# Kernel tuning notes

Hardware: AMD Instinct MI355X
Metric: run time of the kernel (lower is better)

The kernel has to match this reference:

```python
import jax, jax.numpy as jnp
import numpy as np

IN, OUT, HID = 1024, 1024, 2048
L = IN + OUT + HID
EPS = 1e-12  # F.normalize default eps


def _make_strength_matrix():
    fwd_s, bwd_s, lat_s, self_s = 1.0, 0.5, 0.3, 0.0
    i = np.arange(L)
    # torch: triu (incl diag) = forward, then tril (incl diag) = backward -> diag ends up backward here
    A = np.where(i[:, None] >= i[None, :], bwd_s, fwd_s).astype(np.float32)
    # lateral blocks (within input, within output, within hidden)
    A[0:IN, 0:IN] = lat_s
    A[IN:IN + OUT, IN:IN + OUT] = lat_s
    A[IN + OUT:L, IN + OUT:L] = lat_s
    A[i, i] = self_s
    return A


def setup_inputs() -> dict:
    key = jax.random.key(0)
    kx, ky, kw = jax.random.split(key, 3)
    B = 1024
    x = jax.random.normal(kx, (B, IN), dtype=jnp.float32)
    y = jax.random.normal(ky, (B, OUT), dtype=jnp.float32)
    W = jax.random.normal(kw, (L, L), dtype=jnp.float32) * 0.01
    idx = jnp.arange(L)
    W = W.at[idx, idx].set(0.0)  # fill_diagonal_(0) at init
    A = jnp.asarray(_make_strength_matrix())
    return {"x": x, "y": y, "W": W, "A": A, "n": 32}


def reference(x, y, W, A, n):
    # clamp_x=True, clamp_y=False, norm_hidden=True, average_window<=0
    B = x.shape[0]
    act0 = jnp.concatenate(
        [x, jnp.zeros_like(y), jnp.zeros((B, HID), dtype=x.dtype)], axis=1
    )  # [B, L]
    mw = W * A.T  # modified weights, loop-invariant

    def step(act, _):
        act = jax.nn.relu(act @ mw.T)          # linear(act, mw) + relu
        act = act.at[:, :IN].set(x)            # clamp_x
        hid = act[:, IN + OUT:]
        nrm = jnp.linalg.norm(hid, axis=1, keepdims=True)
        hid = hid / jnp.maximum(nrm, EPS)      # F.normalize p=2 dim=1
        act = act.at[:, IN + OUT:].set(hid)
        return act, None

    act, _ = jax.lax.scan(step, act0, None, length=n)
    return act
```

## Files before the change

kernel.cpp:

```cpp
#include <hip/hip_runtime.h>
#include <stdint.h>
#include <stddef.h>


#define L 4096
#define INX 1024
#define OUTX 1024
#define BATCH 1024
#define NCOL 3072
#define NITER 32

#define BM 64
#define BN 96
#define BK 64

typedef float floatx4 __attribute__((ext_vector_type(4)));
typedef short bf16x8 __attribute__((ext_vector_type(8)));

__device__ __forceinline__ unsigned short f2bf(float f) {
  unsigned int u = __float_as_uint(f);
  u += 0x7FFF + ((u >> 16) & 1);
  return (unsigned short)(u >> 16);
}
__device__ __forceinline__ float bf2f(unsigned short h) {
  return __uint_as_float(((unsigned int)h) << 16);
}

__device__ __forceinline__ void load_lds_16B(const void* g, void* s) {
  __builtin_amdgcn_global_load_lds(
      (const __attribute__((address_space(1))) unsigned int*)g,
      (__attribute__((address_space(3))) unsigned int*)s, 16, 0, 0);
}

__global__ void prep_mwn(const float* __restrict__ W, unsigned short* __restrict__ mwn) {
  int idx = blockIdx.x * 256 + threadIdx.x;
  int i = idx >> 10;
  int j4 = (idx & 1023) << 2;
  const float4 w = *(const float4*)&W[(size_t)(INX + i) * L + j4];
  const int c = INX + i;
  const int rc = (c < 2048) ? 1 : 2;
  float wv[4] = {w.x, w.y, w.z, w.w};
  unsigned short o[4];
#pragma unroll
  for (int k = 0; k < 4; ++k) {
    int j = j4 + k;
    int rj = (j < 1024) ? 0 : ((j < 2048) ? 1 : 2);
    float a = (j == c) ? 0.0f : ((rj == rc) ? 0.3f : ((j >= c) ? 0.5f : 1.0f));
    o[k] = f2bf(wv[k] * a);
  }
  *(ushort4*)&mwn[(size_t)i * L + j4] = make_ushort4(o[0], o[1], o[2], o[3]);
}

__global__ void init_act(const float* __restrict__ x, unsigned short* __restrict__ actA) {
  int i = blockIdx.x * 256 + threadIdx.x;
  int col = i & (L - 1), row = i >> 12;
  actA[i] = (col < INX) ? f2bf(x[(size_t)row * INX + col]) : (unsigned short)0;
}

__device__ __forceinline__ void stage(unsigned short* As, unsigned short* Bs,
                                      const unsigned short* gA, const unsigned short* gB,
                                      int kb, int t) {
  const int srow = t >> 3, schunk = t & 7;
  const int o = srow * BK + schunk * 8;
  load_lds_16B(gA + kb, &As[o]);
  load_lds_16B(gA + (size_t)32 * L + kb, &As[o + 32 * BK]);
  load_lds_16B(gB + kb, &Bs[o]);
  load_lds_16B(gB + (size_t)32 * L + kb, &Bs[o + 32 * BK]);
  load_lds_16B(gB + (size_t)64 * L + kb, &Bs[o + 64 * BK]);
}

__device__ __forceinline__ void mfma_step(const unsigned short* As, const unsigned short* Bs,
                                          int wm, int wn, int l15, int quad,
                                          floatx4 acc[2][3]) {
#pragma unroll
  for (int kk = 0; kk < 2; ++kk) {
    bf16x8 af[2], bfr[3];
    const int c = kk * 4 + quad;
#pragma unroll
    for (int mt = 0; mt < 2; ++mt) {
      int r = wm + mt * 16 + l15;
      af[mt] = *(const bf16x8*)&As[r * BK + ((c ^ (r & 7)) * 8)];
    }
#pragma unroll
    for (int nt = 0; nt < 3; ++nt) {
      int r = wn + nt * 16 + l15;
      bfr[nt] = *(const bf16x8*)&Bs[r * BK + ((c ^ (r & 7)) * 8)];
    }
#pragma unroll
    for (int mt = 0; mt < 2; ++mt)
#pragma unroll
      for (int nt = 0; nt < 3; ++nt)
        acc[mt][nt] = __builtin_amdgcn_mfma_f32_16x16x32_bf16(af[mt], bfr[nt],
                                                              acc[mt][nt], 0, 0, 0);
  }
}

#define PSTEP(s, R, D, ACC)                                                       \
  do {                                                                            \
    if ((s) < NS - 1) asm volatile("s_waitcnt vmcnt(5)" ::: "memory");            \
    else              asm volatile("s_waitcnt vmcnt(0)" ::: "memory");            \
    asm volatile("s_barrier" ::: "memory");                                       \
    if ((s) + 2 < NS) stage(As##D, Bs##D, gA, gB, KB0 + ((s) + 2) * BK, t);       \
    mfma_step(As##R, Bs##R, wm, wn, l15, quad, ACC);                              \
  } while (0)

template<int MODE>
__global__ __launch_bounds__(256, 2) void gemm_k(
    const unsigned short* __restrict__ act,
    const unsigned short* __restrict__ mwn,
    unsigned short* __restrict__ actn,
    unsigned short* __restrict__ c0,
    const float* __restrict__ nsq_prev,
    float* __restrict__ nsq_next) {
  __shared__ alignas(16) unsigned short As0[BM * BK], As1[BM * BK], As2[BM * BK];
  __shared__ alignas(16) unsigned short Bs0[BN * BK], Bs1[BN * BK], Bs2[BN * BK];
  const int t = threadIdx.x;
  const int lane = t & 63;
  const int wave = t >> 6;
  const int wm = (wave & 1) * 32;
  const int wn = (wave >> 1) * 48;
  const int l15 = lane & 15;
  const int quad = lane >> 4;

  const int b = blockIdx.y * 32 + blockIdx.x;
  const int n_idx = (b & 7) * 4 + (b >> 7);
  const int m_idx = (b >> 3) & 15;
  const int m0 = m_idx * BM;
  const int n0 = n_idx * BN;

  const int srow = t >> 3;
  const int schunk = t & 7;
  const int gchunk = schunk ^ (srow & 7);
  const unsigned short* gA = act + (size_t)(m0 + srow) * L + gchunk * 8;
  const unsigned short* gB = mwn + (size_t)(n0 + srow) * L + gchunk * 8;

  const int KB0 = MODE ? INX : 0;
  constexpr int NS = MODE ? 48 : 16;

  floatx4 accA[2][3], accB[2][3];
#pragma unroll
  for (int i = 0; i < 2; ++i)
#pragma unroll
    for (int j = 0; j < 3; ++j) {
      accA[i][j] = (floatx4){0.f, 0.f, 0.f, 0.f};
      if (MODE) accB[i][j] = (floatx4){0.f, 0.f, 0.f, 0.f};
    }

  stage(As0, Bs0, gA, gB, KB0, t);
  stage(As1, Bs1, gA, gB, KB0 + BK, t);

  PSTEP(0, 0, 2, accA);  PSTEP(1, 1, 0, accA);  PSTEP(2, 2, 1, accA);
  PSTEP(3, 0, 2, accA);  PSTEP(4, 1, 0, accA);  PSTEP(5, 2, 1, accA);
  PSTEP(6, 0, 2, accA);  PSTEP(7, 1, 0, accA);  PSTEP(8, 2, 1, accA);
  PSTEP(9, 0, 2, accA);  PSTEP(10, 1, 0, accA); PSTEP(11, 2, 1, accA);
  PSTEP(12, 0, 2, accA); PSTEP(13, 1, 0, accA); PSTEP(14, 2, 1, accA);
  PSTEP(15, 0, 2, accA);
  if (MODE) {
    PSTEP(16, 1, 0, accB); PSTEP(17, 2, 1, accB); PSTEP(18, 0, 2, accB);
    PSTEP(19, 1, 0, accB); PSTEP(20, 2, 1, accB); PSTEP(21, 0, 2, accB);
    PSTEP(22, 1, 0, accB); PSTEP(23, 2, 1, accB); PSTEP(24, 0, 2, accB);
    PSTEP(25, 1, 0, accB); PSTEP(26, 2, 1, accB); PSTEP(27, 0, 2, accB);
    PSTEP(28, 1, 0, accB); PSTEP(29, 2, 1, accB); PSTEP(30, 0, 2, accB);
    PSTEP(31, 1, 0, accB); PSTEP(32, 2, 1, accB); PSTEP(33, 0, 2, accB);
    PSTEP(34, 1, 0, accB); PSTEP(35, 2, 1, accB); PSTEP(36, 0, 2, accB);
    PSTEP(37, 1, 0, accB); PSTEP(38, 2, 1, accB); PSTEP(39, 0, 2, accB);
    PSTEP(40, 1, 0, accB); PSTEP(41, 2, 1, accB); PSTEP(42, 0, 2, accB);
    PSTEP(43, 1, 0, accB); PSTEP(44, 2, 1, accB); PSTEP(45, 0, 2, accB);
    PSTEP(46, 1, 0, accB); PSTEP(47, 2, 1, accB);
  }

  if (MODE == 0) {
#pragma unroll
    for (int mt = 0; mt < 2; ++mt)
#pragma unroll
      for (int nt = 0; nt < 3; ++nt) {
        const int gn = n0 + wn + nt * 16 + l15;
#pragma unroll
        for (int r = 0; r < 4; ++r) {
          const int gm = m0 + wm + mt * 16 + quad * 4 + r;
          c0[(size_t)gm * NCOL + gn] = f2bf(accA[mt][nt][r]);
        }
      }
    return;
  }

  float sm[2][4];
#pragma unroll
  for (int mt = 0; mt < 2; ++mt)
#pragma unroll
    for (int r = 0; r < 4; ++r) {
      const int gm = m0 + wm + mt * 16 + quad * 4 + r;
      sm[mt][r] = 1.0f / fmaxf(sqrtf(nsq_prev[gm]), 1e-12f);
    }

  const bool has_hid = (n0 + BN) > OUTX;
#pragma unroll
  for (int mt = 0; mt < 2; ++mt) {
    float ss[4] = {0.f, 0.f, 0.f, 0.f};
#pragma unroll
    for (int nt = 0; nt < 3; ++nt) {
      const int gn = n0 + wn + nt * 16 + l15;
      const bool hid = gn >= OUTX;
#pragma unroll
      for (int r = 0; r < 4; ++r) {
        const int gm = m0 + wm + mt * 16 + quad * 4 + r;
        float v = bf2f(c0[(size_t)gm * NCOL + gn]) + accA[mt][nt][r]
                  + sm[mt][r] * accB[mt][nt][r];
        v = fmaxf(v, 0.f);
        actn[(size_t)gm * L + INX + gn] = f2bf(v);
        if (hid) ss[r] += v * v;
      }
    }
    if (has_hid) {
#pragma unroll
      for (int r = 0; r < 4; ++r) {
        float sv = ss[r];
        sv += __shfl_xor(sv, 1);
        sv += __shfl_xor(sv, 2);
        sv += __shfl_xor(sv, 4);
        sv += __shfl_xor(sv, 8);
        if (l15 == 0)
          atomicAdd(&nsq_next[m0 + wm + mt * 16 + quad * 4 + r], sv);
      }
    }
  }
}

__global__ void finalize(const float* __restrict__ x, const unsigned short* __restrict__ act,
                         const float* __restrict__ nsq_fin, float* __restrict__ out) {
  int i = blockIdx.x * 256 + threadIdx.x;
  int col = i & (L - 1), row = i >> 12;
  float v;
  if (col < INX) {
    v = x[(size_t)row * INX + col];
  } else {
    v = bf2f(act[i]);
    if (col >= INX + OUTX) v *= 1.0f / fmaxf(sqrtf(nsq_fin[row]), 1e-12f);
  }
  out[i] = v;
}

extern "C" void kernel_launch(void* const* d_in, const int* in_sizes, int n_in,
                              void* d_out, int out_size, void* d_ws, size_t ws_size,
                              hipStream_t stream) {
  const float* x = (const float*)d_in[0];
  const float* W = (const float*)d_in[2];
  float* out = (float*)d_out;

  char* ws = (char*)d_ws;
  unsigned short* mwn  = (unsigned short*)(ws);
  unsigned short* actA = (unsigned short*)(ws + 25165824);
  unsigned short* actB = (unsigned short*)(ws + 33554432);
  unsigned short* c0   = (unsigned short*)(ws + 41943040);
  float* normsq        = (float*)(ws + 48234496);

  hipMemsetAsync(normsq, 0, (NITER + 1) * BATCH * sizeof(float), stream);
  prep_mwn<<<(NCOL * (L / 4)) / 256, 256, 0, stream>>>(W, mwn);
  init_act<<<(BATCH * L) / 256, 256, 0, stream>>>(x, actA);

  gemm_k<0><<<dim3(NCOL / BN, BATCH / BM), 256, 0, stream>>>(actA, mwn, nullptr, c0,
                                                             nullptr, nullptr);

  unsigned short* cur = actA;
  unsigned short* nxt = actB;
  for (int it = 0; it < NITER; ++it) {
    gemm_k<1><<<dim3(NCOL / BN, BATCH / BM), 256, 0, stream>>>(
        cur, mwn, nxt, c0, normsq + it * BATCH, normsq + (it + 1) * BATCH);
    unsigned short* tmp = cur; cur = nxt; nxt = tmp;
  }
  finalize<<<(BATCH * L) / 256, 256, 0, stream>>>(x, cur, normsq + NITER * BATCH, out);
}
```

Measured before the change: 1.089 ms.

## Load B operand directly from global into registers, bypassing LDS staging

Each wave now reads its weight (B) fragments straight from global memory into registers in MFMA layout, and only the activation (A) tile is staged through triple-buffered LDS. This removes B's LDS writes and reads and cuts shared-memory use from about 61 KB to about 24 KB per block. The waitcnt is lowered because only two async loads per stage remain. In exchange, the B loads are issued in the same step that consumes them with no prefetch, so global latency is exposed. B rows are also fetched separately by the two waves that share them, which doubles that traffic through the cache.

```diff
diff --git a/kernel.cpp b/kernel.cpp
--- a/kernel.cpp
+++ b/kernel.cpp
@@ -57,51 +57,57 @@
   actA[i] = (col < INX) ? f2bf(x[(size_t)row * INX + col]) : (unsigned short)0;
 }
 
-__device__ __forceinline__ void stage(unsigned short* As, unsigned short* Bs,
-                                      const unsigned short* gA, const unsigned short* gB,
-                                      int kb, int t) {
-  const int srow = t >> 3, schunk = t & 7;
-  const int o = srow * BK + schunk * 8;
+__device__ __forceinline__ void stageA(unsigned short* As, const unsigned short* gA,
+                                       int kb, int t) {
+  const int o = (t >> 3) * BK + (t & 7) * 8;
   load_lds_16B(gA + kb, &As[o]);
   load_lds_16B(gA + (size_t)32 * L + kb, &As[o + 32 * BK]);
-  load_lds_16B(gB + kb, &Bs[o]);
-  load_lds_16B(gB + (size_t)32 * L + kb, &Bs[o + 32 * BK]);
-  load_lds_16B(gB + (size_t)64 * L + kb, &Bs[o + 64 * BK]);
-}
-
-__device__ __forceinline__ void mfma_step(const unsigned short* As, const unsigned short* Bs,
-                                          int wm, int wn, int l15, int quad,
-                                          floatx4 acc[2][3]) {
+}
+
+__device__ __forceinline__ void loadB(bf16x8 b[2][3], const unsigned short* gB0,
+                                      const unsigned short* gB1, const unsigned short* gB2,
+                                      int kb) {
 #pragma unroll
   for (int kk = 0; kk < 2; ++kk) {
-    bf16x8 af[2], bfr[3];
-    const int c = kk * 4 + quad;
+    b[kk][0] = *(const bf16x8*)(gB0 + kb + kk * 32);
+    b[kk][1] = *(const bf16x8*)(gB1 + kb + kk * 32);
+    b[kk][2] = *(const bf16x8*)(gB2 + kb + kk * 32);
+  }
+}
+
+__device__ __forceinline__ void loadA(bf16x8 a[2][2], const unsigned short* As,
+                                      int wm, int l15, int quad) {
+#pragma unroll
+  for (int kk = 0; kk < 2; ++kk)
 #pragma unroll
     for (int mt = 0; mt < 2; ++mt) {
       int r = wm + mt * 16 + l15;
-      af[mt] = *(const bf16x8*)&As[r * BK + ((c ^ (r & 7)) * 8)];
-    }
-#pragma unroll
-    for (int nt = 0; nt < 3; ++nt) {
-      int r = wn + nt * 16 + l15;
-      bfr[nt] = *(const bf16x8*)&Bs[r * BK + ((c ^ (r & 7)) * 8)];
-    }
+      a[kk][mt] = *(const bf16x8*)&As[r * BK + ((((kk * 4 + quad)) ^ (r & 7)) * 8)];
+    }
+}
+
+__device__ __forceinline__ void domfma(const bf16x8 a[2][2], const bf16x8 b[2][3],
+                                       floatx4 acc[2][3]) {
+#pragma unroll
+  for (int kk = 0; kk < 2; ++kk)
 #pragma unroll
     for (int mt = 0; mt < 2; ++mt)
 #pragma unroll
       for (int nt = 0; nt < 3; ++nt)
-        acc[mt][nt] = __builtin_amdgcn_mfma_f32_16x16x32_bf16(af[mt], bfr[nt],
+        acc[mt][nt] = __builtin_amdgcn_mfma_f32_16x16x32_bf16(a[kk][mt], b[kk][nt],
                                                               acc[mt][nt], 0, 0, 0);
-  }
 }
 
 #define PSTEP(s, R, D, ACC)                                                       \
   do {                                                                            \
-    if ((s) < NS - 1) asm volatile("s_waitcnt vmcnt(5)" ::: "memory");            \
+    if ((s) < NS - 1) asm volatile("s_waitcnt vmcnt(2)" ::: "memory");            \
     else              asm volatile("s_waitcnt vmcnt(0)" ::: "memory");            \
     asm volatile("s_barrier" ::: "memory");                                       \
-    if ((s) + 2 < NS) stage(As##D, Bs##D, gA, gB, KB0 + ((s) + 2) * BK, t);       \
-    mfma_step(As##R, Bs##R, wm, wn, l15, quad, ACC);                              \
+    bf16x8 bf[2][3], af[2][2];                                                    \
+    loadB(bf, gB0, gB1, gB2, KB0 + (s) * BK);                                     \
+    loadA(af, As##R, wm, l15, quad);                                              \
+    if ((s) + 2 < NS) stageA(As##D, gA, KB0 + ((s) + 2) * BK, t);                 \
+    domfma(af, bf, ACC);                                                          \
   } while (0)
 
 template<int MODE>
@@ -113,7 +119,6 @@
     const float* __restrict__ nsq_prev,
     float* __restrict__ nsq_next) {
   __shared__ alignas(16) unsigned short As0[BM * BK], As1[BM * BK], As2[BM * BK];
-  __shared__ alignas(16) unsigned short Bs0[BN * BK], Bs1[BN * BK], Bs2[BN * BK];
   const int t = threadIdx.x;
   const int lane = t & 63;
   const int wave = t >> 6;
@@ -129,10 +134,12 @@
   const int n0 = n_idx * BN;
 
   const int srow = t >> 3;
-  const int schunk = t & 7;
-  const int gchunk = schunk ^ (srow & 7);
+  const int gchunk = (t & 7) ^ (srow & 7);
   const unsigned short* gA = act + (size_t)(m0 + srow) * L + gchunk * 8;
-  const unsigned short* gB = mwn + (size_t)(n0 + srow) * L + gchunk * 8;
+
+  const unsigned short* gB0 = mwn + (size_t)(n0 + wn + 0 + l15) * L + quad * 8;
+  const unsigned short* gB1 = mwn + (size_t)(n0 + wn + 16 + l15) * L + quad * 8;
+  const unsigned short* gB2 = mwn + (size_t)(n0 + wn + 32 + l15) * L + quad * 8;
 
   const int KB0 = MODE ? INX : 0;
   constexpr int NS = MODE ? 48 : 16;
@@ -146,8 +153,8 @@
       if (MODE) accB[i][j] = (floatx4){0.f, 0.f, 0.f, 0.f};
     }
 
-  stage(As0, Bs0, gA, gB, KB0, t);
-  stage(As1, Bs1, gA, gB, KB0 + BK, t);
+  stageA(As0, gA, KB0, t);
+  stageA(As1, gA, KB0 + BK, t);
 
   PSTEP(0, 0, 2, accA);  PSTEP(1, 1, 0, accA);  PSTEP(2, 2, 1, accA);
   PSTEP(3, 0, 2, accA);  PSTEP(4, 1, 0, accA);  PSTEP(5, 2, 1, accA);
```

Result: slower. 2.678 ms (+146.0%).

## Double M tile and split K across wave halves with LDS reduction

Applied to the files above, without the earlier changes.

The GEMM block tile grows from 64x96 to 128x96 and uses 512 threads. The two halves of the waves each take half of every K-slice, and their partial accumulators are summed through shared memory at the end. This raises operand reuse per staged tile and halves the grid to 256 blocks, one per CU, to cut redundant loads of the weight matrix. In exchange it adds LDS reduction passes with extra barriers and lowers occupancy to one block per CU.

```diff
diff --git a/kernel.cpp b/kernel.cpp
--- a/kernel.cpp
+++ b/kernel.cpp
@@ -10,7 +10,7 @@
 #define NCOL 3072
 #define NITER 32
 
-#define BM 64
+#define BM 128
 #define BN 96
 #define BK 64
 
@@ -60,94 +60,102 @@
 __device__ __forceinline__ void stage(unsigned short* As, unsigned short* Bs,
                                       const unsigned short* gA, const unsigned short* gB,
                                       int kb, int t) {
-  const int srow = t >> 3, schunk = t & 7;
-  const int o = srow * BK + schunk * 8;
-  load_lds_16B(gA + kb, &As[o]);
-  load_lds_16B(gA + (size_t)32 * L + kb, &As[o + 32 * BK]);
-  load_lds_16B(gB + kb, &Bs[o]);
-  load_lds_16B(gB + (size_t)32 * L + kb, &Bs[o + 32 * BK]);
-  load_lds_16B(gB + (size_t)64 * L + kb, &Bs[o + 64 * BK]);
+  const int o = t * 8;
+  load_lds_16B(gA + kb, As + o);
+  load_lds_16B(gA + (size_t)64 * L + kb, As + 4096 + o);
+  load_lds_16B(gB + kb, Bs + o);
+  if (t < 256)
+    load_lds_16B(gB + (size_t)64 * L + kb, Bs + 4096 + o);
 }
 
 __device__ __forceinline__ void mfma_step(const unsigned short* As, const unsigned short* Bs,
-                                          int wm, int wn, int l15, int quad,
-                                          floatx4 acc[2][3]) {
-#pragma unroll
-  for (int kk = 0; kk < 2; ++kk) {
-    bf16x8 af[2], bfr[3];
-    const int c = kk * 4 + quad;
-#pragma unroll
-    for (int mt = 0; mt < 2; ++mt) {
-      int r = wm + mt * 16 + l15;
-      af[mt] = *(const bf16x8*)&As[r * BK + ((c ^ (r & 7)) * 8)];
-    }
-#pragma unroll
-    for (int nt = 0; nt < 3; ++nt) {
-      int r = wn + nt * 16 + l15;
-      bfr[nt] = *(const bf16x8*)&Bs[r * BK + ((c ^ (r & 7)) * 8)];
-    }
-#pragma unroll
-    for (int mt = 0; mt < 2; ++mt)
-#pragma unroll
-      for (int nt = 0; nt < 3; ++nt)
-        acc[mt][nt] = __builtin_amdgcn_mfma_f32_16x16x32_bf16(af[mt], bfr[nt],
-                                                              acc[mt][nt], 0, 0, 0);
-  }
-}
-
-#define PSTEP(s, R, D, ACC)                                                       \
-  do {                                                                            \
-    if ((s) < NS - 1) asm volatile("s_waitcnt vmcnt(5)" ::: "memory");            \
-    else              asm volatile("s_waitcnt vmcnt(0)" ::: "memory");            \
-    asm volatile("s_barrier" ::: "memory");                                       \
-    if ((s) + 2 < NS) stage(As##D, Bs##D, gA, gB, KB0 + ((s) + 2) * BK, t);       \
-    mfma_step(As##R, Bs##R, wm, wn, l15, quad, ACC);                              \
+                                          int wm, int wn, int ckh, int l15,
+                                          floatx4 acc[4][3]) {
+  bf16x8 af[4], bfr[3];
+#pragma unroll
+  for (int mt = 0; mt < 4; ++mt) {
+    int r = wm + mt * 16 + l15;
+    af[mt] = *(const bf16x8*)&As[r * BK + ((ckh ^ (r & 7)) * 8)];
+  }
+#pragma unroll
+  for (int nt = 0; nt < 3; ++nt) {
+    int r = wn + nt * 16 + l15;
+    bfr[nt] = *(const bf16x8*)&Bs[r * BK + ((ckh ^ (r & 7)) * 8)];
+  }
+#pragma unroll
+  for (int mt = 0; mt < 4; ++mt)
+#pragma unroll
+    for (int nt = 0; nt < 3; ++nt)
+      acc[mt][nt] = __builtin_amdgcn_mfma_f32_16x16x32_bf16(af[mt], bfr[nt],
+                                                            acc[mt][nt], 0, 0, 0);
+}
+
+#define PSTEP(s, R, D, ACC)                                                     \
+  do {                                                                          \
+    if ((s) < NS - 1) {                                                         \
+      if (lowB) asm volatile("s_waitcnt vmcnt(4)" ::: "memory");                \
+      else      asm volatile("s_waitcnt vmcnt(3)" ::: "memory");                \
+    } else {                                                                    \
+      asm volatile("s_waitcnt vmcnt(0)" ::: "memory");                          \
+    }                                                                           \
+    asm volatile("s_barrier" ::: "memory");                                     \
+    if ((s) + 2 < NS) stage(As_##D, Bs_##D, gA, gB, KB0 + ((s) + 2) * BK, t);   \
+    mfma_step(As_##R, Bs_##R, wm, wn, ckh, l15, ACC);                           \
   } while (0)
 
 template<int MODE>
-__global__ __launch_bounds__(256, 2) void gemm_k(
+__global__ __launch_bounds__(512, 1) void gemm_k(
     const unsigned short* __restrict__ act,
     const unsigned short* __restrict__ mwn,
     unsigned short* __restrict__ actn,
     unsigned short* __restrict__ c0,
     const float* __restrict__ nsq_prev,
     float* __restrict__ nsq_next) {
-  __shared__ alignas(16) unsigned short As0[BM * BK], As1[BM * BK], As2[BM * BK];
-  __shared__ alignas(16) unsigned short Bs0[BN * BK], Bs1[BN * BK], Bs2[BN * BK];
+  __shared__ alignas(16) unsigned short SM[43008];
+  unsigned short* const As_0 = SM;
+  unsigned short* const As_1 = SM + 8192;
+  unsigned short* const As_2 = SM + 16384;
+  unsigned short* const Bs_0 = SM + 24576;
+  unsigned short* const Bs_1 = SM + 30720;
+  unsigned short* const Bs_2 = SM + 36864;
+
   const int t = threadIdx.x;
   const int lane = t & 63;
   const int wave = t >> 6;
-  const int wm = (wave & 1) * 32;
-  const int wn = (wave >> 1) * 48;
+  const int pos = wave & 3;
+  const int khalf = wave >> 2;
+  const int wm = (pos & 1) * 64;
+  const int wn = (pos >> 1) * 48;
   const int l15 = lane & 15;
   const int quad = lane >> 4;
+  const int ckh = khalf * 4 + quad;
+  const bool lowB = (t < 256);
 
   const int b = blockIdx.y * 32 + blockIdx.x;
-  const int n_idx = (b & 7) * 4 + (b >> 7);
-  const int m_idx = (b >> 3) & 15;
+  const int n_idx = (b & 7) * 4 + (b >> 6);
+  const int m_idx = (b >> 3) & 7;
   const int m0 = m_idx * BM;
   const int n0 = n_idx * BN;
 
   const int srow = t >> 3;
-  const int schunk = t & 7;
-  const int gchunk = schunk ^ (srow & 7);
+  const int gchunk = (t & 7) ^ (srow & 7);
   const unsigned short* gA = act + (size_t)(m0 + srow) * L + gchunk * 8;
   const unsigned short* gB = mwn + (size_t)(n0 + srow) * L + gchunk * 8;
 
   const int KB0 = MODE ? INX : 0;
   constexpr int NS = MODE ? 48 : 16;
 
-  floatx4 accA[2][3], accB[2][3];
-#pragma unroll
-  for (int i = 0; i < 2; ++i)
+  floatx4 accA[4][3], accB[4][3];
+#pragma unroll
+  for (int i = 0; i < 4; ++i)
 #pragma unroll
     for (int j = 0; j < 3; ++j) {
       accA[i][j] = (floatx4){0.f, 0.f, 0.f, 0.f};
       if (MODE) accB[i][j] = (floatx4){0.f, 0.f, 0.f, 0.f};
     }
 
-  stage(As0, Bs0, gA, gB, KB0, t);
-  stage(As1, Bs1, gA, gB, KB0 + BK, t);
+  stage(As_0, Bs_0, gA, gB, KB0, t);
+  stage(As_1, Bs_1, gA, gB, KB0 + BK, t);
 
   PSTEP(0, 0, 2, accA);  PSTEP(1, 1, 0, accA);  PSTEP(2, 2, 1, accA);
   PSTEP(3, 0, 2, accA);  PSTEP(4, 1, 0, accA);  PSTEP(5, 2, 1, accA);
@@ -169,9 +177,46 @@
     PSTEP(46, 1, 0, accB); PSTEP(47, 2, 1, accB);
   }
 
+  __syncthreads();
+  floatx4* red = (floatx4*)SM;
+  if (khalf) {
+#pragma unroll
+    for (int mt = 0; mt < 4; ++mt)
+#pragma unroll
+      for (int nt = 0; nt < 3; ++nt)
+        red[(mt * 3 + nt) * 256 + pos * 64 + lane] = accA[mt][nt];
+  }
+  __syncthreads();
+  if (!khalf) {
+#pragma unroll
+    for (int mt = 0; mt < 4; ++mt)
+#pragma unroll
+      for (int nt = 0; nt < 3; ++nt)
+        accA[mt][nt] += red[(mt * 3 + nt) * 256 + pos * 64 + lane];
+  }
+  if (MODE) {
+    __syncthreads();
+    if (khalf) {
+#pragma unroll
+      for (int mt = 0; mt < 4; ++mt)
+#pragma unroll
+        for (int nt = 0; nt < 3; ++nt)
+          red[(mt * 3 + nt) * 256 + pos * 64 + lane] = accB[mt][nt];
+    }
+    __syncthreads();
+    if (!khalf) {
+#pragma unroll
+      for (int mt = 0; mt < 4; ++mt)
+#pragma unroll
+        for (int nt = 0; nt < 3; ++nt)
+          accB[mt][nt] += red[(mt * 3 + nt) * 256 + pos * 64 + lane];
+    }
+  }
+  if (khalf) return;
+
   if (MODE == 0) {
 #pragma unroll
-    for (int mt = 0; mt < 2; ++mt)
+    for (int mt = 0; mt < 4; ++mt)
 #pragma unroll
       for (int nt = 0; nt < 3; ++nt) {
         const int gn = n0 + wn + nt * 16 + l15;
@@ -184,9 +229,9 @@
     return;
   }
 
-  float sm[2][4];
-#pragma unroll
-  for (int mt = 0; mt < 2; ++mt)
+  float sm[4][4];
+#pragma unroll
+  for (int mt = 0; mt < 4; ++mt)
 #pragma unroll
     for (int r = 0; r < 4; ++r) {
       const int gm = m0 + wm + mt * 16 + quad * 4 + r;
@@ -195,7 +240,7 @@
 
   const bool has_hid = (n0 + BN) > OUTX;
 #pragma unroll
-  for (int mt = 0; mt < 2; ++mt) {
+  for (int mt = 0; mt < 4; ++mt) {
     float ss[4] = {0.f, 0.f, 0.f, 0.f};
 #pragma unroll
     for (int nt = 0; nt < 3; ++nt) {
@@ -258,13 +303,12 @@
   prep_mwn<<<(NCOL * (L / 4)) / 256, 256, 0, stream>>>(W, mwn);
   init_act<<<(BATCH * L) / 256, 256, 0, stream>>>(x, actA);
 
-  gemm_k<0><<<dim3(NCOL / BN, BATCH / BM), 256, 0, stream>>>(actA, mwn, nullptr, c0,
-                                                             nullptr, nullptr);
+  gemm_k<0><<<dim3(32, 8), 512, 0, stream>>>(actA, mwn, nullptr, c0, nullptr, nullptr);
 
   unsigned short* cur = actA;
   unsigned short* nxt = actB;
   for (int it = 0; it < NITER; ++it) {
-    gemm_k<1><<<dim3(NCOL / BN, BATCH / BM), 256, 0, stream>>>(
+    gemm_k<1><<<dim3(32, 8), 512, 0, stream>>>(
         cur, mwn, nxt, c0, normsq + it * BATCH, normsq + (it + 1) * BATCH);
     unsigned short* tmp = cur; cur = nxt; nxt = tmp;
   }
```

After: 1.148 ms. 5.4% more time.
